# Performance work log

Measured on AMD Instinct MI355X. Metric: run time of the kernel, lower is better.

Reference implementation:

```python
import jax, jax.numpy as jnp
import numpy as np

B, S, D = 2, 2048, 2048
H, KVH, DH = 16, 4, 128
WIN = 128
THETA = 10000.0  # local rope (layer_idx=0 -> local/sliding path)


def setup_inputs() -> dict:
    key = jax.random.key(0)
    ks = jax.random.split(key, 5)
    return {
        "x": jax.random.normal(ks[0], (B, S, D), dtype=jnp.float32),
        "Wq": jax.random.normal(ks[1], (H * DH, D), dtype=jnp.float32) * 0.02,
        "Wk": jax.random.normal(ks[2], (KVH * DH, D), dtype=jnp.float32) * 0.02,
        "Wv": jax.random.normal(ks[3], (KVH * DH, D), dtype=jnp.float32) * 0.02,
        "Wo": jax.random.normal(ks[4], (D, H * DH), dtype=jnp.float32) * 0.02,
    }


def _rotate_half(t):
    half = t.shape[-1] // 2
    return jnp.concatenate([-t[..., half:], t[..., :half]], axis=-1)


def _rope_tables(seq_len, head_dim, theta, dtype):
    inv_freq = 1.0 / (theta ** (jnp.arange(0, head_dim, 2, dtype=jnp.float32) / head_dim))
    freqs = jnp.arange(seq_len, dtype=jnp.float32)[:, None] * inv_freq[None, :]  # [S, DH/2]
    # source does repeat_interleave(cos, 2, dim=-1): [S, DH]
    cos = jnp.repeat(jnp.cos(freqs), 2, axis=-1).astype(dtype)
    sin = jnp.repeat(jnp.sin(freqs), 2, axis=-1).astype(dtype)
    return cos[None, :, None, :], sin[None, :, None, :]  # broadcast over [B,S,H,DH]


def reference(x, Wq, Wk, Wv, Wo):
    b, s, _ = x.shape
    q = (x @ Wq.T).reshape(b, s, H, DH)
    k = (x @ Wk.T).reshape(b, s, KVH, DH)
    v = (x @ Wv.T).reshape(b, s, KVH, DH)

    cos, sin = _rope_tables(s, DH, THETA, x.dtype)
    q = q * cos + _rotate_half(q) * sin
    k = k * cos + _rotate_half(k) * sin

    # GQA: repeat_interleave kv heads to n_heads
    groups = H // KVH
    k = jnp.repeat(k, groups, axis=2)
    v = jnp.repeat(v, groups, axis=2)

    q = q.transpose(0, 2, 1, 3)  # [B,H,S,DH]
    k = k.transpose(0, 2, 1, 3)
    v = v.transpose(0, 2, 1, 3)

    scale = DH ** -0.5
    scores = jnp.einsum('bhqd,bhkd->bhqk', q, k) * scale  # [B,H,S,S]

    # faithful local mask from source: q_idx >= k_idx - window_size
    iq = jnp.arange(s)[:, None]
    ik = jnp.arange(s)[None, :]
    mask = iq >= (ik - WIN)  # [S,S]
    scores = jnp.where(mask[None, None, :, :], scores, jnp.float32(-jnp.inf).astype(scores.dtype))

    attn = jax.nn.softmax(scores, axis=-1)
    out = jnp.einsum('bhqk,bhkd->bhqd', attn, v)
    out = out.transpose(0, 2, 1, 3).reshape(b, s, H * DH)
    return out @ Wo.T
```

## Files before the change

### kernel.cpp

```cpp
#include <hip/hip_runtime.h>
#include <hip/hip_bf16.h>

using bf16 = __hip_bfloat16;
typedef __attribute__((ext_vector_type(8))) short short8;
typedef __attribute__((ext_vector_type(4))) float floatx4;

#define AS1 __attribute__((address_space(1)))
#define AS3 __attribute__((address_space(3)))

__device__ __forceinline__ floatx4 mfma16(short8 a, short8 b, floatx4 c) {
  return __builtin_amdgcn_mfma_f32_16x16x32_bf16(a, b, c, 0, 0, 0);
}
__device__ __forceinline__ void gload16(const bf16* g, bf16* l) {
  __builtin_amdgcn_global_load_lds((const AS1 unsigned*)g, (AS3 unsigned*)l, 16, 0, 0);
}
__device__ __forceinline__ unsigned pk_bf16(float lo, float hi) {
  unsigned r;
  asm("v_cvt_pk_bf16_f32 %0, %1, %2" : "=v"(r) : "v"(lo), "v"(hi));
  return r;
}
__device__ __forceinline__ void swap32(unsigned& a, unsigned& b) {
  asm("v_permlane32_swap_b32 %0, %1" : "+v"(a), "+v"(b));
}
__device__ __forceinline__ void swap16(unsigned& a, unsigned& b) {
  asm("v_permlane16_swap_b32 %0, %1" : "+v"(a), "+v"(b));
}
__device__ __forceinline__ short8 mk_frag(unsigned w0, unsigned w1, unsigned w2,
                                          unsigned w3) {
  union { unsigned w[4]; short8 s; } r;
  r.w[0] = w0; r.w[1] = w1; r.w[2] = w2; r.w[3] = w3;
  return r.s;
}
__device__ __forceinline__ float b2f(unsigned short u) {
  union { float f; unsigned i; } x;
  x.i = ((unsigned)u) << 16;
  return x.f;
}

__global__ void cast_all_k(const float* __restrict__ x, const float* __restrict__ Wq,
                           const float* __restrict__ Wk, const float* __restrict__ Wv,
                           const float* __restrict__ Wo, bf16* __restrict__ xb,
                           bf16* __restrict__ wqkv, bf16* __restrict__ wo_b) {
  int blk = blockIdx.x;
  const float* src;
  bf16* dst;
  int off;
  if (blk < 8192)       { src = x;  dst = xb;                 off = blk; }
  else if (blk < 12288) { src = Wq; dst = wqkv;               off = blk - 8192; }
  else if (blk < 13312) { src = Wk; dst = wqkv + 2048 * 2048; off = blk - 12288; }
  else if (blk < 14336) { src = Wv; dst = wqkv + 2560 * 2048; off = blk - 13312; }
  else                  { src = Wo; dst = wo_b;               off = blk - 14336; }
  int i = (off * 256 + threadIdx.x) * 4;
  float4 v = *(const float4*)(src + i);
  bf16 t[4] = {__float2bfloat16(v.x), __float2bfloat16(v.y),
               __float2bfloat16(v.z), __float2bfloat16(v.w)};
  *(ushort4*)(dst + i) = *(const ushort4*)t;
}

template <typename OutT>
__global__ __launch_bounds__(256, 2)
void gemm_bt(const bf16* __restrict__ A, const bf16* __restrict__ B,
             OutT* __restrict__ C, int M, int N, int K) {
  __shared__ alignas(16) bf16 As[128 * 32];
  __shared__ alignas(16) bf16 Bs[128 * 32];
  const int tid = threadIdx.x;
  const int w = tid >> 6, lane = tid & 63, l16 = lane & 15, quad = lane >> 4;
  const int bm = blockIdx.x << 7, bn = blockIdx.y << 7;
  const int wm = (w & 1) << 6, wn = (w >> 1) << 6;

  const int r = tid >> 2, p = tid & 3;
  const int g0 = (p ^ ((r >> 1) & 3)) << 3;
  const int g1 = (p ^ (((r + 64) >> 1) & 3)) << 3;
  const bf16* Ag0 = A + (long)(bm + r) * K + g0;
  const bf16* Ag1 = A + (long)(bm + r + 64) * K + g1;
  const bf16* Bg0 = B + (long)(bn + r) * K + g0;
  const bf16* Bg1 = B + (long)(bn + r + 64) * K + g1;
  bf16* Asw = As + (w << 9);
  bf16* Bsw = Bs + (w << 9);

  floatx4 acc[4][4];
#pragma unroll
  for (int i = 0; i < 4; ++i)
#pragma unroll
    for (int j = 0; j < 4; ++j) acc[i][j] = (floatx4)(0.0f);

  for (int k0 = 0; k0 < K; k0 += 32) {
    gload16(Ag0 + k0, Asw);
    gload16(Ag1 + k0, Asw + 2048);
    gload16(Bg0 + k0, Bsw);
    gload16(Bg1 + k0, Bsw + 2048);
    __syncthreads();
    short8 af[4], bfv[4];
#pragma unroll
    for (int mi = 0; mi < 4; ++mi) {
      int row = wm + (mi << 4) + l16;
      int pos = quad ^ ((row >> 1) & 3);
      af[mi] = *(const short8*)(As + row * 32 + pos * 8);
    }
#pragma unroll
    for (int ni = 0; ni < 4; ++ni) {
      int row = wn + (ni << 4) + l16;
      int pos = quad ^ ((row >> 1) & 3);
      bfv[ni] = *(const short8*)(Bs + row * 32 + pos * 8);
    }
#pragma unroll
    for (int mi = 0; mi < 4; ++mi)
#pragma unroll
      for (int ni = 0; ni < 4; ++ni)
        acc[mi][ni] = mfma16(af[mi], bfv[ni], acc[mi][ni]);
    __syncthreads();
  }

#pragma unroll
  for (int mi = 0; mi < 4; ++mi)
#pragma unroll
    for (int ni = 0; ni < 4; ++ni)
#pragma unroll
      for (int rr = 0; rr < 4; ++rr) {
        int row = bm + wm + (mi << 4) + (quad << 2) + rr;
        int col = bn + wn + (ni << 4) + l16;
        float v = acc[mi][ni][rr];
        if constexpr (sizeof(OutT) == 2)
          C[(long)row * N + col] = __float2bfloat16(v);
        else
          C[(long)row * N + col] = v;
      }
}

__global__ void rope_k(const bf16* __restrict__ qkv, bf16* __restrict__ Q,
                       bf16* __restrict__ Kd) {
  int idx = blockIdx.x * 256 + threadIdx.x;
  int g = idx & 7;
  int rest = idx >> 3;
  int head = rest % 20;
  int token = rest / 20;
  int s = token & 2047;
  int b = token >> 11;
  int d0 = g << 3;
  const float C0 = 0.20762050593046439f;
  float fs = (float)s;
  float cl[4], sl[4], ch[4], sh[4];
#pragma unroll
  for (int f = 0; f < 4; ++f) {
    float i1 = (float)((d0 >> 1) + f);
    float a1 = fs * exp2f(-i1 * C0);
    float a2 = fs * exp2f(-(i1 + 32.0f) * C0);
    __sincosf(a1, &sl[f], &cl[f]);
    __sincosf(a2, &sh[f], &ch[f]);
  }
  bool isq = head < 16;
  const bf16* p = qkv + (long)token * 3072 +
                  (isq ? head * 128 : 2048 + (head - 16) * 128) + d0;
  union U { short8 v; unsigned short u[8]; } lo, hi, olo, ohi;
  lo.v = *(const short8*)p;
  hi.v = *(const short8*)(p + 64);
  const float sc = isq ? 0.08838834764831845f * 1.4426950408889634f : 1.0f;
#pragma unroll
  for (int i = 0; i < 8; ++i) {
    int f = i >> 1;
    float xl = b2f(lo.u[i]), xh = b2f(hi.u[i]);
    bf16 vlo = __float2bfloat16((xl * cl[f] - xh * sl[f]) * sc);
    bf16 vhi = __float2bfloat16((xh * ch[f] + xl * sh[f]) * sc);
    olo.u[i] = *(const unsigned short*)&vlo;
    ohi.u[i] = *(const unsigned short*)&vhi;
  }
  bf16* dst = isq ? (Q + ((long)((b << 4) + head) * 2048 + s) * 128 + d0)
                  : (Kd + ((long)((b << 2) + (head - 16)) * 2048 + s) * 128 + d0);
  *(short8*)dst = olo.v;
  *(short8*)(dst + 64) = ohi.v;
}

__global__ void vtrans_k(const bf16* __restrict__ qkv, bf16* __restrict__ Vt) {
  __shared__ bf16 t[32][33];
  int x = threadIdx.x, y = threadIdx.y;
  int s0 = blockIdx.x << 5, d0 = blockIdx.y << 5, bkv = blockIdx.z;
  int b = bkv >> 2, kvh = bkv & 3;
  const bf16* src = qkv + (long)((b << 11) + s0) * 3072 + 2560 + kvh * 128 + d0;
#pragma unroll
  for (int yy = y; yy < 32; yy += 8) t[yy][x] = src[(long)yy * 3072 + x];
  __syncthreads();
  bf16* dst = Vt + (long)((bkv << 7) + d0) * 2048 + s0;
#pragma unroll
  for (int yy = y; yy < 32; yy += 8) dst[(long)yy * 2048 + x] = t[x][yy];
}

__global__ __launch_bounds__(256, 2)
void attn_k(const bf16* __restrict__ Q, const bf16* __restrict__ K,
            const bf16* __restrict__ V, bf16* __restrict__ O) {
  __shared__ alignas(16) bf16 lk[2][64 * 128];
  __shared__ alignas(16) bf16 lv[2][128 * 64];
  const int tid = threadIdx.x, w = tid >> 6, lane = tid & 63;
  const int l16 = lane & 15, quad = lane >> 4;
  const int id = blockIdx.x;
  const int xcd = id & 7;
  const int b = xcd >> 2, kvh = xcd & 3;
  const int rem = id >> 3;
  const int bx = rem >> 2;
  const int h = (kvh << 2) | (rem & 3);
  const int bh = (b << 4) | h;
  const int qa0 = bx << 6, qb0 = (31 - bx) << 6;
  const int nkA = bx + 3;
  int nkBt = 34 - bx;
  const int nkB = nkBt < 32 ? nkBt : 32;
  const int jmA = bx + 2, jmB = 33 - bx;
  const bf16* Qp = Q + (long)bh * 2048 * 128;
  const bf16* Kp = K + (long)((b << 2) + kvh) * 2048 * 128;
  const bf16* Vp = V + (long)((b << 2) + kvh) * 128 * 2048;

  short8 qfA[4], qfB[4];
#pragma unroll
  for (int kc = 0; kc < 4; ++kc) {
    qfA[kc] = *(const short8*)(Qp + (long)(qa0 + (w << 4) + l16) * 128 + kc * 32 + quad * 8);
    qfB[kc] = *(const short8*)(Qp + (long)(qb0 + (w << 4) + l16) * 128 + kc * 32 + quad * 8);
  }

  floatx4 oA[8], oB[8];
#pragma unroll
  for (int i = 0; i < 8; ++i) { oA[i] = (floatx4)(0.0f); oB[i] = (floatx4)(0.0f); }
  float lA = 0.0f, lB = 0.0f;

  auto stage = [&](int j, int bufi) {
    const int k0 = j << 6;
    bf16* lkb = &lk[bufi][0];
    bf16* lvb = &lv[bufi][0];
#pragma unroll
    for (int i = 0; i < 4; ++i) {
      int c = i * 256 + tid;
      int row = c >> 4, pos = c & 15;
      int grp = (pos & 8) | ((pos & 7) ^ (row & 7));
      gload16(Kp + (long)(k0 + row) * 128 + grp * 8, lkb + (i * 256 + (w << 6)) * 8);
    }
#pragma unroll
    for (int i = 0; i < 4; ++i) {
      int c = i * 256 + tid;
      int row = c >> 3, grp = (c & 7) ^ (row & 7);
      gload16(Vp + (long)row * 2048 + k0 + grp * 8, lvb + (i * 256 + (w << 6)) * 8);
    }
  };

  auto tile = [&](auto bothc, int k0, bool maskA, bool maskB, int bufi) {
    constexpr bool BOTH = decltype(bothc)::value;
    const bf16* lkb = &lk[bufi][0];
    const bf16* lvb = &lv[bufi][0];
    floatx4 sA[4], sB[4];
#pragma unroll
    for (int kt = 0; kt < 4; ++kt) {
      sB[kt] = (floatx4)(0.0f);
      if constexpr (BOTH) sA[kt] = (floatx4)(0.0f);
    }
    __builtin_amdgcn_s_setprio(1);
#pragma unroll
    for (int kc = 0; kc < 4; ++kc) {
#pragma unroll
      for (int kt = 0; kt < 4; ++kt) {
        int row = (kt << 4) + l16;
        int g = (kc << 2) + quad;
        int pos = (g & 8) | ((g & 7) ^ (row & 7));
        short8 kf = *(const short8*)(lkb + row * 128 + pos * 8);
        sB[kt] = mfma16(kf, qfB[kc], sB[kt]);
        if constexpr (BOTH) sA[kt] = mfma16(kf, qfA[kc], sA[kt]);
      }
    }
    __builtin_amdgcn_s_setprio(0);
    if (maskB) {
      int qg = qb0 + (w << 4) + l16 + 128;
#pragma unroll
      for (int kt = 0; kt < 4; ++kt)
#pragma unroll
        for (int rr = 0; rr < 4; ++rr) {
          int kg = k0 + (kt << 4) + (quad << 2) + rr;
          if (kg > qg) sB[kt][rr] = -1e30f;
        }
    }
    if constexpr (BOTH) {
      if (maskA) {
        int qg = qa0 + (w << 4) + l16 + 128;
#pragma unroll
        for (int kt = 0; kt < 4; ++kt)
#pragma unroll
          for (int rr = 0; rr < 4; ++rr) {
            int kg = k0 + (kt << 4) + (quad << 2) + rr;
            if (kg > qg) sA[kt][rr] = -1e30f;
          }
      }
    }
    unsigned wBp[4][2], wAp[4][2];
#pragma unroll
    for (int kt = 0; kt < 4; ++kt) {
      float p0 = exp2f(sB[kt][0]), p1 = exp2f(sB[kt][1]);
      float p2 = exp2f(sB[kt][2]), p3 = exp2f(sB[kt][3]);
      lB += (p0 + p1) + (p2 + p3);
      wBp[kt][0] = pk_bf16(p0, p1);
      wBp[kt][1] = pk_bf16(p2, p3);
      if constexpr (BOTH) {
        float a0 = exp2f(sA[kt][0]), a1 = exp2f(sA[kt][1]);
        float a2 = exp2f(sA[kt][2]), a3 = exp2f(sA[kt][3]);
        lA += (a0 + a1) + (a2 + a3);
        wAp[kt][0] = pk_bf16(a0, a1);
        wAp[kt][1] = pk_bf16(a2, a3);
      }
    }
#pragma unroll
    for (int kcl = 0; kcl < 2; ++kcl) {
      unsigned a0 = wBp[2 * kcl][0], a1 = wBp[2 * kcl][1];
      unsigned b0 = wBp[2 * kcl + 1][0], b1 = wBp[2 * kcl + 1][1];
      swap32(a0, b0); swap16(a0, b0);
      swap32(a1, b1); swap16(a1, b1);
      short8 pfB = mk_frag(a0, a1, b0, b1);
      short8 pfA;
      if constexpr (BOTH) {
        unsigned c0 = wAp[2 * kcl][0], c1 = wAp[2 * kcl][1];
        unsigned d0 = wAp[2 * kcl + 1][0], d1 = wAp[2 * kcl + 1][1];
        swap32(c0, d0); swap16(c0, d0);
        swap32(c1, d1); swap16(c1, d1);
        pfA = mk_frag(c0, c1, d0, d1);
      }
      int g = (kcl << 2) + quad;
      __builtin_amdgcn_s_setprio(1);
#pragma unroll
      for (int nd = 0; nd < 8; ++nd) {
        int vrow = (nd << 4) + l16;
        int vpos = g ^ (vrow & 7);
        short8 vf = *(const short8*)(lvb + vrow * 64 + (vpos << 3));
        oB[nd] = mfma16(pfB, vf, oB[nd]);
        if constexpr (BOTH) oA[nd] = mfma16(pfA, vf, oA[nd]);
      }
      __builtin_amdgcn_s_setprio(0);
    }
  };

  stage(0, 0);
  __syncthreads();
  for (int j = 0; j < nkB; ++j) {
    if (j + 1 < nkB) stage(j + 1, (j + 1) & 1);
    const int k0 = j << 6;
    if (j < nkA)
      tile(std::integral_constant<bool, true>{}, k0, j == jmA, j == jmB, j & 1);
    else
      tile(std::integral_constant<bool, false>{}, k0, false, j == jmB, j & 1);
    __syncthreads();
  }

  lA += __shfl_xor(lA, 16, 64); lA += __shfl_xor(lA, 32, 64);
  lB += __shfl_xor(lB, 16, 64); lB += __shfl_xor(lB, 32, 64);
  float liA = 1.0f / lA, liB = 1.0f / lB;
  float rlA[4], rlB[4];
#pragma unroll
  for (int rr = 0; rr < 4; ++rr) {
    int src = (quad << 2) + rr;
    rlA[rr] = __shfl(liA, src, 64);
    rlB[rr] = __shfl(liB, src, 64);
  }

  bf16* OpA = O + ((long)(b << 11) + qa0 + (w << 4)) * 2048 + (h << 7);
  bf16* OpB = O + ((long)(b << 11) + qb0 + (w << 4)) * 2048 + (h << 7);
#pragma unroll
  for (int nd = 0; nd < 8; ++nd)
#pragma unroll
    for (int rr = 0; rr < 4; ++rr) {
      int row = (quad << 2) + rr;
      int col = (nd << 4) + l16;
      OpA[(long)row * 2048 + col] = __float2bfloat16(oA[nd][rr] * rlA[rr]);
      OpB[(long)row * 2048 + col] = __float2bfloat16(oB[nd][rr] * rlB[rr]);
    }
}

extern "C" void kernel_launch(void* const* d_in, const int* in_sizes, int n_in,
                              void* d_out, int out_size, void* d_ws, size_t ws_size,
                              hipStream_t stream) {
  (void)in_sizes; (void)n_in; (void)out_size; (void)ws_size;
  const float* x  = (const float*)d_in[0];
  const float* Wq = (const float*)d_in[1];
  const float* Wk = (const float*)d_in[2];
  const float* Wv = (const float*)d_in[3];
  const float* Wo = (const float*)d_in[4];
  char* ws = (char*)d_ws;
  bf16* xb   = (bf16*)(ws);
  bf16* wqkv = (bf16*)(ws + 16777216);
  bf16* wo_b = (bf16*)(ws + 29360128);
  bf16* qkv  = (bf16*)(ws + 37748736);
  bf16* Qr   = (bf16*)(ws + 62914560);
  bf16* Kr   = (bf16*)(ws + 79691776);
  bf16* Vt   = (bf16*)(ws + 83886080);
  bf16* Ob   = xb;
  float* out = (float*)d_out;

  cast_all_k<<<18432, 256, 0, stream>>>(x, Wq, Wk, Wv, Wo, xb, wqkv, wo_b);

  gemm_bt<bf16><<<dim3(32, 24), 256, 0, stream>>>(xb, wqkv, qkv, 4096, 3072, 2048);
  rope_k<<<2560, 256, 0, stream>>>(qkv, Qr, Kr);
  vtrans_k<<<dim3(64, 4, 8), dim3(32, 8), 0, stream>>>(qkv, Vt);
  attn_k<<<dim3(512), 256, 0, stream>>>(Qr, Kr, Vt, Ob);
  gemm_bt<float><<<dim3(32, 16), 256, 0, stream>>>(Ob, wo_b, out, 4096, 2048, 2048);
}
```

Measured before the change: 281.7 us.

## Software-pipeline QK^T of next tile ahead of softmax/PV with triple-buffered K

Splits the attention tile into a QK^T stage and a mask/softmax/PV stage, and computes the score MFMAs for tile j+1 before finishing tile j. K staging moves to a three-deep LDS ring and V stays double-buffered, so K loads run two tiles ahead. The aim is to overlap softmax VALU work with matrix-core work across tiles. In exchange, the extra live score accumulators raise register pressure under the 2-blocks-per-CU launch bound, LDS use grows, and the s_setprio hints are dropped.

```diff
diff --git a/kernel.cpp b/kernel.cpp
--- a/kernel.cpp
+++ b/kernel.cpp
@@ -187,7 +187,7 @@
 __global__ __launch_bounds__(256, 2)
 void attn_k(const bf16* __restrict__ Q, const bf16* __restrict__ K,
             const bf16* __restrict__ V, bf16* __restrict__ O) {
-  __shared__ alignas(16) bf16 lk[2][64 * 128];
+  __shared__ alignas(16) bf16 lk[3][64 * 128];
   __shared__ alignas(16) bf16 lv[2][128 * 64];
   const int tid = threadIdx.x, w = tid >> 6, lane = tid & 63;
   const int l16 = lane & 15, quad = lane >> 4;
@@ -219,10 +219,9 @@
   for (int i = 0; i < 8; ++i) { oA[i] = (floatx4)(0.0f); oB[i] = (floatx4)(0.0f); }
   float lA = 0.0f, lB = 0.0f;
 
-  auto stage = [&](int j, int bufi) {
+  auto stageK = [&](int j, int bufi) {
     const int k0 = j << 6;
     bf16* lkb = &lk[bufi][0];
-    bf16* lvb = &lv[bufi][0];
 #pragma unroll
     for (int i = 0; i < 4; ++i) {
       int c = i * 256 + tid;
@@ -230,6 +229,10 @@
       int grp = (pos & 8) | ((pos & 7) ^ (row & 7));
       gload16(Kp + (long)(k0 + row) * 128 + grp * 8, lkb + (i * 256 + (w << 6)) * 8);
     }
+  };
+  auto stageV = [&](int j, int bufi) {
+    const int k0 = j << 6;
+    bf16* lvb = &lv[bufi][0];
 #pragma unroll
     for (int i = 0; i < 4; ++i) {
       int c = i * 256 + tid;
@@ -238,17 +241,14 @@
     }
   };
 
-  auto tile = [&](auto bothc, int k0, bool maskA, bool maskB, int bufi) {
+  auto qk = [&](auto bothc, int bufi, floatx4* sA, floatx4* sB) {
     constexpr bool BOTH = decltype(bothc)::value;
     const bf16* lkb = &lk[bufi][0];
-    const bf16* lvb = &lv[bufi][0];
-    floatx4 sA[4], sB[4];
 #pragma unroll
     for (int kt = 0; kt < 4; ++kt) {
       sB[kt] = (floatx4)(0.0f);
       if constexpr (BOTH) sA[kt] = (floatx4)(0.0f);
     }
-    __builtin_amdgcn_s_setprio(1);
 #pragma unroll
     for (int kc = 0; kc < 4; ++kc) {
 #pragma unroll
@@ -261,7 +261,12 @@
         if constexpr (BOTH) sA[kt] = mfma16(kf, qfA[kc], sA[kt]);
       }
     }
-    __builtin_amdgcn_s_setprio(0);
+  };
+
+  auto fin = [&](auto bothc, int k0, bool maskA, bool maskB, int vbuf,
+                 floatx4* sA, floatx4* sB) {
+    constexpr bool BOTH = decltype(bothc)::value;
+    const bf16* lvb = &lv[vbuf][0];
     if (maskB) {
       int qg = qb0 + (w << 4) + l16 + 128;
 #pragma unroll
@@ -329,17 +334,35 @@
     }
   };
 
-  stage(0, 0);
+  floatx4 sAc[4], sBc[4], sAn[4], sBn[4];
+  constexpr std::integral_constant<bool, true> T{};
+  constexpr std::integral_constant<bool, false> F{};
+
+  stageK(0, 0);
+  stageV(0, 0);
+  stageK(1, 1);
   __syncthreads();
+  qk(T, 0, sAc, sBc);
+
+  int bq = 2, bs = 2;
   for (int j = 0; j < nkB; ++j) {
-    if (j + 1 < nkB) stage(j + 1, (j + 1) & 1);
+    const int jn = j + 1;
+    if (jn + 1 < nkB) stageK(jn + 1, bs);
+    if (jn < nkB) stageV(jn, jn & 1);
+    if (jn < nkB) {
+      const int bqi = jn == 1 ? 1 : (jn % 3);
+      if (jn < nkA) qk(T, bqi, sAn, sBn);
+      else          qk(F, bqi, sAn, sBn);
+    }
     const int k0 = j << 6;
-    if (j < nkA)
-      tile(std::integral_constant<bool, true>{}, k0, j == jmA, j == jmB, j & 1);
-    else
-      tile(std::integral_constant<bool, false>{}, k0, false, j == jmB, j & 1);
+    if (j < nkA) fin(T, k0, j == jmA, j == jmB, j & 1, sAc, sBc);
+    else         fin(F, k0, false, j == jmB, j & 1, sAc, sBc);
     __syncthreads();
-  }
+#pragma unroll
+    for (int kt = 0; kt < 4; ++kt) { sAc[kt] = sAn[kt]; sBc[kt] = sBn[kt]; }
+    bs = bs == 2 ? 0 : bs + 1;
+  }
+  (void)bq;
 
   lA += __shfl_xor(lA, 16, 64); lA += __shfl_xor(lA, 32, 64);
   lB += __shfl_xor(lB, 16, 64); lB += __shfl_xor(lB, 32, 64);
```

New measurement: 291.5 us. 3.5% more time.

## Add 256x256-tile pipelined GEMM with swizzled LDS for QKV projection

Applied to the files above, without the earlier changes.

Adds a new GEMM kernel using 256x256 output tiles, 512 threads, BK=64, double-buffered LDS filled by direct global-to-LDS loads with an XOR swizzle, and interleaves the next tile's loads with four quarter-tile MFMA phases under explicit barriers and setprio. It replaces the previous 128-tile GEMM only for the QKV projection, aiming for more data reuse per block and overlap of loads with compute. The grid shrinks to 192 blocks, so fewer blocks than CUs may be used, and the hand-placed waitcnt/barrier sequence risks races if the counts are wrong.

```diff
diff --git a/kernel.cpp b/kernel.cpp
--- a/kernel.cpp
+++ b/kernel.cpp
@@ -36,6 +36,9 @@
   x.i = ((unsigned)u) << 16;
   return x.f;
 }
+
+#define BAR() asm volatile("s_barrier" ::: "memory")
+#define VM6() asm volatile("s_waitcnt vmcnt(6)" ::: "memory")
 
 __global__ void cast_all_k(const float* __restrict__ x, const float* __restrict__ Wq,
                            const float* __restrict__ Wk, const float* __restrict__ Wv,
@@ -119,6 +122,133 @@
       for (int rr = 0; rr < 4; ++rr) {
         int row = bm + wm + (mi << 4) + (quad << 2) + rr;
         int col = bn + wn + (ni << 4) + l16;
+        float v = acc[mi][ni][rr];
+        if constexpr (sizeof(OutT) == 2)
+          C[(long)row * N + col] = __float2bfloat16(v);
+        else
+          C[(long)row * N + col] = v;
+      }
+}
+
+template <typename OutT>
+__global__ __launch_bounds__(512, 2)
+void gemm256_bt(const bf16* __restrict__ A, const bf16* __restrict__ B,
+                OutT* __restrict__ C, int M, int N, int K) {
+  __shared__ alignas(16) bf16 lA[2][16384];
+  __shared__ alignas(16) bf16 lB[2][16384];
+  const int tid = threadIdx.x;
+  const int w = tid >> 6, lane = tid & 63, l16 = lane & 15, quad = lane >> 4;
+  const int wm = w >> 2, wn = w & 3;
+  const int bm = blockIdx.x << 8, bn = blockIdx.y << 8;
+  const int NT = K >> 6;
+
+  const int lr3 = lane >> 3;
+  const int ks = ((lane & 7) ^ (lr3 & 7)) << 3;
+  const int j0 = w << 1, j1 = j0 + 1;
+  const int rA00 = ((j0 >> 3) << 7) | ((j0 & 7) << 3);
+  const int rA01 = ((j1 >> 3) << 7) | ((j1 & 7) << 3);
+  const int rA10 = rA00 | 64, rA11 = rA01 | 64;
+  const int rB00 = ((j0 >> 2) << 6) | ((j0 & 3) << 3);
+  const int rB01 = ((j1 >> 2) << 6) | ((j1 & 3) << 3);
+  const int rB10 = rB00 | 32, rB11 = rB01 | 32;
+  const bf16* pA00 = A + (long)(bm + rA00 + lr3) * K + ks;
+  const bf16* pA01 = A + (long)(bm + rA01 + lr3) * K + ks;
+  const bf16* pA10 = A + (long)(bm + rA10 + lr3) * K + ks;
+  const bf16* pA11 = A + (long)(bm + rA11 + lr3) * K + ks;
+  const bf16* pB00 = B + (long)(bn + rB00 + lr3) * K + ks;
+  const bf16* pB01 = B + (long)(bn + rB01 + lr3) * K + ks;
+  const bf16* pB10 = B + (long)(bn + rB10 + lr3) * K + ks;
+  const bf16* pB11 = B + (long)(bn + rB11 + lr3) * K + ks;
+
+  floatx4 acc[8][4];
+#pragma unroll
+  for (int i = 0; i < 8; ++i)
+#pragma unroll
+    for (int j = 0; j < 4; ++j) acc[i][j] = (floatx4)(0.0f);
+
+  auto stA0 = [&](int k0, int nb) {
+    gload16(pA00 + k0, &lA[nb][rA00 << 6]);
+    gload16(pA01 + k0, &lA[nb][rA01 << 6]);
+  };
+  auto stA1 = [&](int k0, int nb) {
+    gload16(pA10 + k0, &lA[nb][rA10 << 6]);
+    gload16(pA11 + k0, &lA[nb][rA11 << 6]);
+  };
+  auto stB0 = [&](int k0, int nb) {
+    gload16(pB00 + k0, &lB[nb][rB00 << 6]);
+    gload16(pB01 + k0, &lB[nb][rB01 << 6]);
+  };
+  auto stB1 = [&](int k0, int nb) {
+    gload16(pB10 + k0, &lB[nb][rB10 << 6]);
+    gload16(pB11 + k0, &lB[nb][rB11 << 6]);
+  };
+
+  short8 af[4][2];
+  const int sw0 = (quad ^ (l16 & 7)) << 3;
+  const int sw1 = ((4 + quad) ^ (l16 & 7)) << 3;
+  auto rdA = [&](int mh, const bf16* la) {
+    const int rb = wm * 128 + mh * 64 + l16;
+#pragma unroll
+    for (int mi = 0; mi < 4; ++mi) {
+      const bf16* p = la + (rb + mi * 16) * 64;
+      af[mi][0] = *(const short8*)(p + sw0);
+      af[mi][1] = *(const short8*)(p + sw1);
+    }
+  };
+  auto rdB = [&](int nh, const bf16* lb, short8 (*bfr)[2]) {
+    const int rb = wn * 64 + nh * 32 + l16;
+#pragma unroll
+    for (int ni = 0; ni < 2; ++ni) {
+      const bf16* p = lb + (rb + ni * 16) * 64;
+      bfr[ni][0] = *(const short8*)(p + sw0);
+      bfr[ni][1] = *(const short8*)(p + sw1);
+    }
+  };
+  auto mm = [&](auto MHc, auto NHc, short8 (*bfr)[2]) {
+    constexpr int MH4 = decltype(MHc)::value * 4;
+    constexpr int NH2 = decltype(NHc)::value * 2;
+    __builtin_amdgcn_s_setprio(1);
+#pragma unroll
+    for (int kc = 0; kc < 2; ++kc)
+#pragma unroll
+      for (int mi = 0; mi < 4; ++mi)
+#pragma unroll
+        for (int ni = 0; ni < 2; ++ni)
+          acc[MH4 + mi][NH2 + ni] =
+              mfma16(af[mi][kc], bfr[ni][kc], acc[MH4 + mi][NH2 + ni]);
+    __builtin_amdgcn_s_setprio(0);
+  };
+
+  constexpr std::integral_constant<int, 0> I0{};
+  constexpr std::integral_constant<int, 1> I1{};
+
+  stA0(0, 0); stB0(0, 0); stB1(0, 0); stA1(0, 0);
+
+  for (int t = 0; t < NT; ++t) {
+    const int buf = t & 1, nb = buf ^ 1;
+    const int k0n = (t + 1 < NT) ? ((t + 1) << 6) : 0;
+    const bf16* la = &lA[buf][0];
+    const bf16* lb = &lB[buf][0];
+    short8 bf0[2][2], bf1[2][2];
+    stA0(k0n, nb); VM6(); BAR();
+    rdA(0, la); rdB(0, lb, bf0); mm(I0, I0, bf0);
+    stB0(k0n, nb); VM6(); BAR();
+    rdB(1, lb, bf1); mm(I0, I1, bf1);
+    stB1(k0n, nb); VM6(); BAR();
+    rdA(1, la); mm(I1, I1, bf1);
+    stA1(k0n, nb); BAR();
+    rdB(0, lb, bf0); mm(I1, I0, bf0);
+  }
+  asm volatile("s_waitcnt vmcnt(0)" ::: "memory");
+
+#pragma unroll
+  for (int mi = 0; mi < 8; ++mi)
+#pragma unroll
+    for (int ni = 0; ni < 4; ++ni)
+#pragma unroll
+      for (int rr = 0; rr < 4; ++rr) {
+        int row = bm + wm * 128 + mi * 16 + (quad << 2) + rr;
+        int col = bn + wn * 64 + ni * 16 + l16;
         float v = acc[mi][ni][rr];
         if constexpr (sizeof(OutT) == 2)
           C[(long)row * N + col] = __float2bfloat16(v);
@@ -387,7 +517,7 @@
 
   cast_all_k<<<18432, 256, 0, stream>>>(x, Wq, Wk, Wv, Wo, xb, wqkv, wo_b);
 
-  gemm_bt<bf16><<<dim3(32, 24), 256, 0, stream>>>(xb, wqkv, qkv, 4096, 3072, 2048);
+  gemm256_bt<bf16><<<dim3(16, 12), 512, 0, stream>>>(xb, wqkv, qkv, 4096, 3072, 2048);
   rope_k<<<2560, 256, 0, stream>>>(qkv, Qr, Kr);
   vtrans_k<<<dim3(64, 4, 8), dim3(32, 8), 0, stream>>>(qkv, Vt);
   attn_k<<<dim3(512), 256, 0, stream>>>(Qr, Kr, Vt, Ob);
```

Result: slower. 299.5 us (+6.3%).

## Split attention blocks to one query tile each with 32-key tiles

Applied to the files above, without the earlier changes.

Each attention block now processes one 64-row query tile instead of a paired short/long tile, so the grid doubles to 1024 blocks. Key tiles shrink from 64 to 32 rows, which halves LDS use and lets occupancy rise from 2 to 4 blocks per CU. Each wave stops at its own causal limit, but stays in the loop for barriers. This trades the old load balancing from pairing tiles for more parallelism and finer masking, at the cost of more barriers per key and fewer MFMAs per LDS load.

```diff
diff --git a/kernel.cpp b/kernel.cpp
--- a/kernel.cpp
+++ b/kernel.cpp
@@ -184,184 +184,139 @@
   for (int yy = y; yy < 32; yy += 8) dst[(long)yy * 2048 + x] = t[x][yy];
 }
 
-__global__ __launch_bounds__(256, 2)
+__global__ __launch_bounds__(256, 4)
 void attn_k(const bf16* __restrict__ Q, const bf16* __restrict__ K,
             const bf16* __restrict__ V, bf16* __restrict__ O) {
-  __shared__ alignas(16) bf16 lk[2][64 * 128];
-  __shared__ alignas(16) bf16 lv[2][128 * 64];
-  const int tid = threadIdx.x, w = tid >> 6, lane = tid & 63;
+  __shared__ alignas(16) bf16 lk[2][32 * 128];
+  __shared__ alignas(16) bf16 lv[2][128 * 32];
+  const int tid = threadIdx.x, wl = tid >> 6, lane = tid & 63;
   const int l16 = lane & 15, quad = lane >> 4;
   const int id = blockIdx.x;
   const int xcd = id & 7;
   const int b = xcd >> 2, kvh = xcd & 3;
-  const int rem = id >> 3;
-  const int bx = rem >> 2;
-  const int h = (kvh << 2) | (rem & 3);
+  const int rest = id >> 3;
+  const int h = (kvh << 2) | (rest & 3);
+  const int u = rest >> 2;
+  const int t = (u & 1) ? (31 - (u >> 1)) : (u >> 1);
   const int bh = (b << 4) | h;
-  const int qa0 = bx << 6, qb0 = (31 - bx) << 6;
-  const int nkA = bx + 3;
-  int nkBt = 34 - bx;
-  const int nkB = nkBt < 32 ? nkBt : 32;
-  const int jmA = bx + 2, jmB = 33 - bx;
+  const int q0 = t << 6;
+  int nkMt = 2 * t + 6;
+  const int nkMax = nkMt < 64 ? nkMt : 64;
+  int nkwt = 2 * t + 5 + (wl >> 1);
+  const int nk_w = nkwt < 64 ? nkwt : 64;
+  const int jm = 2 * t + 4 + (wl >> 1);
   const bf16* Qp = Q + (long)bh * 2048 * 128;
   const bf16* Kp = K + (long)((b << 2) + kvh) * 2048 * 128;
   const bf16* Vp = V + (long)((b << 2) + kvh) * 128 * 2048;
 
-  short8 qfA[4], qfB[4];
-#pragma unroll
-  for (int kc = 0; kc < 4; ++kc) {
-    qfA[kc] = *(const short8*)(Qp + (long)(qa0 + (w << 4) + l16) * 128 + kc * 32 + quad * 8);
-    qfB[kc] = *(const short8*)(Qp + (long)(qb0 + (w << 4) + l16) * 128 + kc * 32 + quad * 8);
-  }
-
-  floatx4 oA[8], oB[8];
-#pragma unroll
-  for (int i = 0; i < 8; ++i) { oA[i] = (floatx4)(0.0f); oB[i] = (floatx4)(0.0f); }
-  float lA = 0.0f, lB = 0.0f;
+  short8 qf[4];
+#pragma unroll
+  for (int kc = 0; kc < 4; ++kc)
+    qf[kc] = *(const short8*)(Qp + (long)(q0 + (wl << 4) + l16) * 128 + kc * 32 + quad * 8);
+
+  floatx4 oA[8];
+#pragma unroll
+  for (int i = 0; i < 8; ++i) oA[i] = (floatx4)(0.0f);
+  float lA = 0.0f;
 
   auto stage = [&](int j, int bufi) {
-    const int k0 = j << 6;
+    const int k0 = j << 5;
     bf16* lkb = &lk[bufi][0];
     bf16* lvb = &lv[bufi][0];
 #pragma unroll
-    for (int i = 0; i < 4; ++i) {
+    for (int i = 0; i < 2; ++i) {
       int c = i * 256 + tid;
       int row = c >> 4, pos = c & 15;
       int grp = (pos & 8) | ((pos & 7) ^ (row & 7));
-      gload16(Kp + (long)(k0 + row) * 128 + grp * 8, lkb + (i * 256 + (w << 6)) * 8);
-    }
-#pragma unroll
-    for (int i = 0; i < 4; ++i) {
+      gload16(Kp + (long)(k0 + row) * 128 + grp * 8, lkb + (i * 256 + (wl << 6)) * 8);
+    }
+#pragma unroll
+    for (int i = 0; i < 2; ++i) {
       int c = i * 256 + tid;
-      int row = c >> 3, grp = (c & 7) ^ (row & 7);
-      gload16(Vp + (long)row * 2048 + k0 + grp * 8, lvb + (i * 256 + (w << 6)) * 8);
+      int row = c >> 2, cg = c & 3;
+      int grp = cg ^ (row & 3) ^ ((row >> 2) & 3);
+      gload16(Vp + (long)row * 2048 + k0 + grp * 8, lvb + (i * 256 + (wl << 6)) * 8);
     }
   };
 
-  auto tile = [&](auto bothc, int k0, bool maskA, bool maskB, int bufi) {
-    constexpr bool BOTH = decltype(bothc)::value;
+  auto tile = [&](int k0, bool maskT, int bufi) {
     const bf16* lkb = &lk[bufi][0];
     const bf16* lvb = &lv[bufi][0];
-    floatx4 sA[4], sB[4];
-#pragma unroll
-    for (int kt = 0; kt < 4; ++kt) {
-      sB[kt] = (floatx4)(0.0f);
-      if constexpr (BOTH) sA[kt] = (floatx4)(0.0f);
-    }
+    floatx4 sA[2];
+    sA[0] = (floatx4)(0.0f);
+    sA[1] = (floatx4)(0.0f);
     __builtin_amdgcn_s_setprio(1);
 #pragma unroll
     for (int kc = 0; kc < 4; ++kc) {
 #pragma unroll
-      for (int kt = 0; kt < 4; ++kt) {
+      for (int kt = 0; kt < 2; ++kt) {
         int row = (kt << 4) + l16;
         int g = (kc << 2) + quad;
         int pos = (g & 8) | ((g & 7) ^ (row & 7));
         short8 kf = *(const short8*)(lkb + row * 128 + pos * 8);
-        sB[kt] = mfma16(kf, qfB[kc], sB[kt]);
-        if constexpr (BOTH) sA[kt] = mfma16(kf, qfA[kc], sA[kt]);
+        sA[kt] = mfma16(kf, qf[kc], sA[kt]);
       }
     }
     __builtin_amdgcn_s_setprio(0);
-    if (maskB) {
-      int qg = qb0 + (w << 4) + l16 + 128;
-#pragma unroll
-      for (int kt = 0; kt < 4; ++kt)
+    if (maskT) {
+      int qg = q0 + (wl << 4) + l16 + 128;
+#pragma unroll
+      for (int kt = 0; kt < 2; ++kt)
 #pragma unroll
         for (int rr = 0; rr < 4; ++rr) {
           int kg = k0 + (kt << 4) + (quad << 2) + rr;
-          if (kg > qg) sB[kt][rr] = -1e30f;
+          if (kg > qg) sA[kt][rr] = -1e30f;
         }
     }
-    if constexpr (BOTH) {
-      if (maskA) {
-        int qg = qa0 + (w << 4) + l16 + 128;
-#pragma unroll
-        for (int kt = 0; kt < 4; ++kt)
-#pragma unroll
-          for (int rr = 0; rr < 4; ++rr) {
-            int kg = k0 + (kt << 4) + (quad << 2) + rr;
-            if (kg > qg) sA[kt][rr] = -1e30f;
-          }
-      }
-    }
-    unsigned wBp[4][2], wAp[4][2];
-#pragma unroll
-    for (int kt = 0; kt < 4; ++kt) {
-      float p0 = exp2f(sB[kt][0]), p1 = exp2f(sB[kt][1]);
-      float p2 = exp2f(sB[kt][2]), p3 = exp2f(sB[kt][3]);
-      lB += (p0 + p1) + (p2 + p3);
-      wBp[kt][0] = pk_bf16(p0, p1);
-      wBp[kt][1] = pk_bf16(p2, p3);
-      if constexpr (BOTH) {
-        float a0 = exp2f(sA[kt][0]), a1 = exp2f(sA[kt][1]);
-        float a2 = exp2f(sA[kt][2]), a3 = exp2f(sA[kt][3]);
-        lA += (a0 + a1) + (a2 + a3);
-        wAp[kt][0] = pk_bf16(a0, a1);
-        wAp[kt][1] = pk_bf16(a2, a3);
-      }
-    }
-#pragma unroll
-    for (int kcl = 0; kcl < 2; ++kcl) {
-      unsigned a0 = wBp[2 * kcl][0], a1 = wBp[2 * kcl][1];
-      unsigned b0 = wBp[2 * kcl + 1][0], b1 = wBp[2 * kcl + 1][1];
-      swap32(a0, b0); swap16(a0, b0);
-      swap32(a1, b1); swap16(a1, b1);
-      short8 pfB = mk_frag(a0, a1, b0, b1);
-      short8 pfA;
-      if constexpr (BOTH) {
-        unsigned c0 = wAp[2 * kcl][0], c1 = wAp[2 * kcl][1];
-        unsigned d0 = wAp[2 * kcl + 1][0], d1 = wAp[2 * kcl + 1][1];
-        swap32(c0, d0); swap16(c0, d0);
-        swap32(c1, d1); swap16(c1, d1);
-        pfA = mk_frag(c0, c1, d0, d1);
-      }
-      int g = (kcl << 2) + quad;
-      __builtin_amdgcn_s_setprio(1);
-#pragma unroll
-      for (int nd = 0; nd < 8; ++nd) {
-        int vrow = (nd << 4) + l16;
-        int vpos = g ^ (vrow & 7);
-        short8 vf = *(const short8*)(lvb + vrow * 64 + (vpos << 3));
-        oB[nd] = mfma16(pfB, vf, oB[nd]);
-        if constexpr (BOTH) oA[nd] = mfma16(pfA, vf, oA[nd]);
-      }
-      __builtin_amdgcn_s_setprio(0);
-    }
+    unsigned wAp[2][2];
+#pragma unroll
+    for (int kt = 0; kt < 2; ++kt) {
+      float p0 = exp2f(sA[kt][0]), p1 = exp2f(sA[kt][1]);
+      float p2 = exp2f(sA[kt][2]), p3 = exp2f(sA[kt][3]);
+      lA += (p0 + p1) + (p2 + p3);
+      wAp[kt][0] = pk_bf16(p0, p1);
+      wAp[kt][1] = pk_bf16(p2, p3);
+    }
+    unsigned a0 = wAp[0][0], a1 = wAp[0][1];
+    unsigned b0 = wAp[1][0], b1 = wAp[1][1];
+    swap32(a0, b0); swap16(a0, b0);
+    swap32(a1, b1); swap16(a1, b1);
+    short8 pf = mk_frag(a0, a1, b0, b1);
+    __builtin_amdgcn_s_setprio(1);
+#pragma unroll
+    for (int nd = 0; nd < 8; ++nd) {
+      int vrow = (nd << 4) + l16;
+      int vpos = quad ^ (vrow & 3) ^ ((vrow >> 2) & 3);
+      short8 vf = *(const short8*)(lvb + vrow * 32 + (vpos << 3));
+      oA[nd] = mfma16(pf, vf, oA[nd]);
+    }
+    __builtin_amdgcn_s_setprio(0);
   };
 
   stage(0, 0);
   __syncthreads();
-  for (int j = 0; j < nkB; ++j) {
-    if (j + 1 < nkB) stage(j + 1, (j + 1) & 1);
-    const int k0 = j << 6;
-    if (j < nkA)
-      tile(std::integral_constant<bool, true>{}, k0, j == jmA, j == jmB, j & 1);
-    else
-      tile(std::integral_constant<bool, false>{}, k0, false, j == jmB, j & 1);
+  for (int j = 0; j < nkMax; ++j) {
+    if (j + 1 < nkMax) stage(j + 1, (j + 1) & 1);
+    if (j < nk_w)
+      tile(j << 5, j >= jm, j & 1);
     __syncthreads();
   }
 
-  lA += __shfl_xor(lA, 16, 64); lA += __shfl_xor(lA, 32, 64);
-  lB += __shfl_xor(lB, 16, 64); lB += __shfl_xor(lB, 32, 64);
-  float liA = 1.0f / lA, liB = 1.0f / lB;
-  float rlA[4], rlB[4];
-#pragma unroll
-  for (int rr = 0; rr < 4; ++rr) {
-    int src = (quad << 2) + rr;
-    rlA[rr] = __shfl(liA, src, 64);
-    rlB[rr] = __shfl(liB, src, 64);
-  }
-
-  bf16* OpA = O + ((long)(b << 11) + qa0 + (w << 4)) * 2048 + (h << 7);
-  bf16* OpB = O + ((long)(b << 11) + qb0 + (w << 4)) * 2048 + (h << 7);
+  lA += __shfl_xor(lA, 16, 64);
+  lA += __shfl_xor(lA, 32, 64);
+  float liA = 1.0f / lA;
+  float rlA[4];
+#pragma unroll
+  for (int rr = 0; rr < 4; ++rr) rlA[rr] = __shfl(liA, (quad << 2) + rr, 64);
+
+  bf16* Op = O + ((long)(b << 11) + q0 + (wl << 4)) * 2048 + (h << 7);
 #pragma unroll
   for (int nd = 0; nd < 8; ++nd)
 #pragma unroll
     for (int rr = 0; rr < 4; ++rr) {
       int row = (quad << 2) + rr;
       int col = (nd << 4) + l16;
-      OpA[(long)row * 2048 + col] = __float2bfloat16(oA[nd][rr] * rlA[rr]);
-      OpB[(long)row * 2048 + col] = __float2bfloat16(oB[nd][rr] * rlB[rr]);
+      Op[(long)row * 2048 + col] = __float2bfloat16(oA[nd][rr] * rlA[rr]);
     }
 }
 
@@ -390,6 +345,6 @@
   gemm_bt<bf16><<<dim3(32, 24), 256, 0, stream>>>(xb, wqkv, qkv, 4096, 3072, 2048);
   rope_k<<<2560, 256, 0, stream>>>(qkv, Qr, Kr);
   vtrans_k<<<dim3(64, 4, 8), dim3(32, 8), 0, stream>>>(qkv, Vt);
-  attn_k<<<dim3(512), 256, 0, stream>>>(Qr, Kr, Vt, Ob);
+  attn_k<<<dim3(1024), 256, 0, stream>>>(Qr, Kr, Vt, Ob);
   gemm_bt<float><<<dim3(32, 16), 256, 0, stream>>>(Ob, wo_b, out, 4096, 2048, 2048);
 }
```

Result: slower. 303.2 us (+7.6%).
